# Optimization experiments

Measured on AMD Instinct MI355X. Metric: run time of the kernel, lower is better.

The kernel has to match this reference:

```python
import jax, jax.numpy as jnp
import numpy as np

NEG_SLOPE = 0.2  # LeakyReLU slope

N, E, D_IN, D_OUT, H, NBIN = 50000, 500000, 256, 256, 8, 10
DH = D_OUT // H


def setup_inputs() -> dict:
    key = jax.random.key(0)
    ks = jax.random.split(key, 9)
    emb_rel = jax.random.normal(ks[0], (N, D_IN), dtype=jnp.float32)
    head_idxs = jax.random.randint(ks[1], (E,), 0, N, dtype=jnp.int32)
    tail_idxs = jax.random.randint(ks[2], (E,), 0, N, dtype=jnp.int32)
    bins = jax.random.randint(ks[3], (E,), 0, NBIN, dtype=jnp.int32)
    # xavier-normal-ish scaled params (gain for relu)
    attn_proj_w = jax.random.normal(ks[4], (D_OUT, 2 * D_IN), dtype=jnp.float32) * (1.4142 * (2.0 / (2 * D_IN + D_OUT)) ** 0.5)
    attn_proj_b = jnp.zeros((D_OUT,), dtype=jnp.float32)
    attn_bin = jax.random.normal(ks[5], (NBIN, H, 1), dtype=jnp.float32) * 0.3
    attn_vec = jax.random.normal(ks[6], (1, H, DH), dtype=jnp.float32) * (1.4142 * (2.0 / (H + DH)) ** 0.5)
    aggr_proj_w = jax.random.normal(ks[7], (D_OUT, D_IN), dtype=jnp.float32) * (1.4142 * (2.0 / (D_IN + D_OUT)) ** 0.5)
    aggr_proj_b = jnp.zeros((D_OUT,), dtype=jnp.float32)
    return {
        "emb_rel": emb_rel,
        "head_idxs": head_idxs,
        "tail_idxs": tail_idxs,
        "bins": bins,
        "attn_proj_w": attn_proj_w,
        "attn_proj_b": attn_proj_b,
        "attn_bin": attn_bin,
        "attn_vec": attn_vec,
        "aggr_proj_w": aggr_proj_w,
        "aggr_proj_b": aggr_proj_b,
        "num_nodes": N,
    }


def reference(emb_rel, head_idxs, tail_idxs, bins, attn_proj_w, attn_proj_b,
              attn_bin, attn_vec, aggr_proj_w, aggr_proj_b, num_nodes):
    num_head, dim_hid = attn_vec.shape[1], attn_vec.shape[2]
    eh = emb_rel[head_idxs]                      # (E, D_in)
    et = emb_rel[tail_idxs]                      # (E, D_in)
    concat = jnp.concatenate([eh, et], axis=-1)  # (E, 2*D_in)
    proj = (concat @ attn_proj_w.T + attn_proj_b).reshape(-1, num_head, dim_hid)
    lrelu = jnp.where(proj >= 0, proj, NEG_SLOPE * proj)
    # raw attention logits per edge/head: (E, H, 1)
    attn_raw = jnp.sum(lrelu * attn_vec, axis=-1, keepdims=True) + attn_bin[bins]
    # segmented softmax over edges grouped by head node
    seg_max = jax.ops.segment_max(attn_raw, head_idxs, num_segments=num_nodes)
    seg_max = jnp.where(jnp.isfinite(seg_max), seg_max, 0.0)  # empty segments -> 0 (never gathered anyway)
    attn_val = jnp.exp(attn_raw - seg_max[head_idxs])
    attn_sums = jax.ops.segment_sum(attn_val, head_idxs, num_segments=num_nodes)
    beta = attn_val / (attn_sums[head_idxs] + 1e-16)            # (E, H, 1)
    aggr = (et @ aggr_proj_w.T + aggr_proj_b).reshape(-1, num_head, dim_hid)
    out = jax.ops.segment_sum(beta * aggr, head_idxs, num_segments=num_nodes)
    return out.reshape(num_nodes, num_head * dim_hid)
```

## Files before the change

### kernel.cpp

```cpp
#include <hip/hip_runtime.h>
#include <math.h>

#define D_IN 256
#define D_OUT 256
#define NH 8
#define DH 32
#define NBIN 10
#define NEG_SLOPE 0.2f
#define CAP 96
#define LOG2E 1.4426950408889634f
#define THR 8.0f

typedef short short8 __attribute__((ext_vector_type(8)));
typedef float f32x4 __attribute__((ext_vector_type(4)));

__device__ __forceinline__ unsigned short f2bf(float f) {
  unsigned u = __float_as_uint(f);
  unsigned r = u + 0x7fffu + ((u >> 16) & 1u);
  return (unsigned short)(r >> 16);
}
__device__ __forceinline__ float bf2f(unsigned short s) {
  return __uint_as_float((unsigned)s << 16);
}

__device__ __forceinline__ void gload16(const void* g, void* l) {
  __builtin_amdgcn_global_load_lds(
      (const __attribute__((address_space(1))) unsigned int*)g,
      (__attribute__((address_space(3))) unsigned int*)l, 16, 0, 0);
}

__global__ void prep_kernel(const float* __restrict__ attn_w,
                            const float* __restrict__ attn_b,
                            const float* __restrict__ aggr_w,
                            const float* __restrict__ aggr_b,
                            const float* __restrict__ emb,
                            unsigned short* __restrict__ WCbf,
                            float* __restrict__ biasC,
                            unsigned short* __restrict__ embbf,
                            int* __restrict__ cnt, int N) {
  const int b = blockIdx.x, k = threadIdx.x;
  if (b < 768) {
    const int j = b;
    int idx0 = j * 256 + k;
    if (idx0 < N) cnt[idx0] = 0;
    float v, bia = 0.f;
    if (j < 256) {
      v = attn_w[j * 512 + k];
    } else {
      int idx = j - 256, g = idx >> 3, r = idx & 7;
      if (r < 4) { int c = g * 4 + r;     v = attn_w[c * 512 + 256 + k]; bia = attn_b[c]; }
      else       { int c = g * 4 + r - 4; v = aggr_w[c * 256 + k];       bia = aggr_b[c]; }
    }
    WCbf[j * 256 + k] = f2bf(v);
    if (k == 0) biasC[j] = bia;
  } else {
    const long long total = (long long)N * 256;
    long long i = (((long long)(b - 768)) * 256 + k) * 8;
    if (i >= total) return;
    float4 a = *(const float4*)(emb + i);
    float4 c = *(const float4*)(emb + i + 4);
    short8 o;
    o[0] = (short)f2bf(a.x); o[1] = (short)f2bf(a.y);
    o[2] = (short)f2bf(a.z); o[3] = (short)f2bf(a.w);
    o[4] = (short)f2bf(c.x); o[5] = (short)f2bf(c.y);
    o[6] = (short)f2bf(c.z); o[7] = (short)f2bf(c.w);
    *(short8*)(embbf + i) = o;
  }
}

#define EPAD 36
__global__ __launch_bounds__(256) void gemm_bf16_kernel(
    const unsigned short* __restrict__ Abf,
    const unsigned short* __restrict__ Bbf,
    const float* __restrict__ biasC,
    float* __restrict__ P1, unsigned short* __restrict__ P2A, int N) {
  __shared__ char smem[32768];
  float* Ls = (float*)smem;
  const int tid = threadIdx.x;
  const int row0 = blockIdx.x * 128, col0 = blockIdx.y * 128;
  const int wave = tid >> 6, l = tid & 63;
  const int wm = wave >> 1, wn = wave & 1;
  const int lr = l & 15;
  const int lq = l >> 4;
  const int srow = tid >> 2;
  const int sk = (tid & 3) * 8;
  int ar0 = row0 + srow;      if (ar0 >= N) ar0 = N - 1;
  int ar1 = row0 + 64 + srow; if (ar1 >= N) ar1 = N - 1;
  const unsigned short* pa0 = Abf + (size_t)ar0 * 256 + sk;
  const unsigned short* pa1 = Abf + (size_t)ar1 * 256 + sk;
  const unsigned short* pb0 = Bbf + (size_t)(col0 + srow) * 256 + sk;
  const unsigned short* pb1 = Bbf + (size_t)(col0 + 64 + srow) * 256 + sk;

  auto STAGE = [&](int buf, int kk) {
    unsigned short* base = (unsigned short*)(smem + buf * 16384);
    gload16(pa0 + kk, base + wave * 512);
    gload16(pa1 + kk, base + 2048 + wave * 512);
    gload16(pb0 + kk, base + 4096 + wave * 512);
    gload16(pb1 + kk, base + 6144 + wave * 512);
  };

  f32x4 acc[4][4] = {};
  STAGE(0, 0);
  __syncthreads();
  int cur = 0;
  for (int t = 0; t < 8; ++t) {
    if (t < 7) STAGE(cur ^ 1, (t + 1) * 32);
    __builtin_amdgcn_sched_barrier(0);
    const unsigned short* As = (const unsigned short*)(smem + cur * 16384);
    const unsigned short* Bs = As + 4096;
    short8 af[4], bfr[4];
#pragma unroll
    for (int i = 0; i < 4; ++i)
      af[i] = *(const short8*)&As[(wm * 64 + i * 16 + lr) * 32 + lq * 8];
#pragma unroll
    for (int j = 0; j < 4; ++j)
      bfr[j] = *(const short8*)&Bs[(wn * 64 + j * 16 + lr) * 32 + lq * 8];
#pragma unroll
    for (int i = 0; i < 4; ++i)
#pragma unroll
      for (int j = 0; j < 4; ++j)
        acc[i][j] = __builtin_amdgcn_mfma_f32_16x16x32_bf16(af[i], bfr[j], acc[i][j], 0, 0, 0);
    __syncthreads();
    cur ^= 1;
  }
  for (int j = 0; j < 4; ++j) {
    __syncthreads();
    const float bias = biasC[col0 + wn * 64 + j * 16 + lr];
#pragma unroll
    for (int i = 0; i < 4; ++i) {
      const int lrow = wm * 64 + i * 16 + lq * 4;
#pragma unroll
      for (int r = 0; r < 4; ++r)
        Ls[(lrow + r) * EPAD + wn * 16 + lr] = acc[i][j][r] + bias;
    }
    __syncthreads();
    if (col0 < 256) {
      const int sub = tid & 7, half = sub >> 2, quad = sub & 3;
#pragma unroll
      for (int s = 0; s < 4; ++s) {
        const int row = (tid >> 3) + s * 32;
        const int grow = row0 + row;
        if (grow < N) {
          float4 v = *(const float4*)&Ls[row * EPAD + half * 16 + quad * 4];
          *(float4*)(P1 + (size_t)grow * 256 + col0 + half * 64 + j * 16 + quad * 4) = v;
        }
      }
    } else {
      const int o = tid & 3, half = o >> 1, part = o & 1;
#pragma unroll
      for (int s = 0; s < 2; ++s) {
        const int row = (tid >> 2) + s * 64;
        const int grow = row0 + row;
        if (grow < N) {
          const float* src = &Ls[row * EPAD + half * 16 + part * 8];
          short8 v;
#pragma unroll
          for (int q = 0; q < 8; ++q) v[q] = (short)f2bf(src[q]);
          *(short8*)(P2A + (size_t)grow * 512 + (col0 - 256) + half * 64 + j * 16 + part * 8) = v;
        }
      }
    }
  }
}

__global__ void bucket_scatter_kernel(const int* __restrict__ head,
                                      const int* __restrict__ tail,
                                      const int* __restrict__ bins,
                                      int* __restrict__ cnt,
                                      int* __restrict__ bucket, int E) {
  int e = blockIdx.x * blockDim.x + threadIdx.x;
  if (e >= E) return;
  int h = head[e];
  int slot = atomicAdd(&cnt[h], 1);
  if (slot < CAP) bucket[(size_t)h * CAP + slot] = (bins[e] << 16) | tail[e];
}

template <int PAT>
__device__ __forceinline__ float swz_add(float s) {
  return s + __uint_as_float(
      (unsigned)__builtin_amdgcn_ds_swizzle((int)__float_as_uint(s), PAT));
}

__device__ __forceinline__ short8 ldP2A(const unsigned short* __restrict__ P2A,
                                        int t, int l8) {
  return *(const short8*)(P2A + ((size_t)(t & 0xFFFF) << 9) + l8);
}

__device__ __forceinline__ float edge_dot(short8 c, float4 p1, float4 av) {
  float x, s;
  x = p1.x + bf2f((unsigned short)c[0]); s  = fmaxf(x, NEG_SLOPE * x) * av.x;
  x = p1.y + bf2f((unsigned short)c[1]); s += fmaxf(x, NEG_SLOPE * x) * av.y;
  x = p1.z + bf2f((unsigned short)c[2]); s += fmaxf(x, NEG_SLOPE * x) * av.z;
  x = p1.w + bf2f((unsigned short)c[3]); s += fmaxf(x, NEG_SLOPE * x) * av.w;
  s = swz_add<0x041F>(s);
  s = swz_add<0x081F>(s);
  s = swz_add<0x101F>(s);
  return s;
}

__device__ __forceinline__ float4 edge_val(short8 c) {
  float4 v;
  v.x = bf2f((unsigned short)c[4]); v.y = bf2f((unsigned short)c[5]);
  v.z = bf2f((unsigned short)c[6]); v.w = bf2f((unsigned short)c[7]);
  return v;
}

__global__ __launch_bounds__(128) void node_aggr_kernel(
    const float* __restrict__ P1, const unsigned short* __restrict__ P2A,
    const int* __restrict__ cnt, const int* __restrict__ bucket,
    const float* __restrict__ attn_vec, const float* __restrict__ attn_bin,
    float* __restrict__ out, int N) {
  __shared__ float sbin[NBIN * NH];
  const int tid = threadIdx.x;
  if (tid < NBIN * NH) sbin[tid] = attn_bin[tid] * LOG2E;
  __syncthreads();
  const int nu = __builtin_amdgcn_readfirstlane(blockIdx.x * 2 + (tid >> 6));
  if (nu >= N) return;
  const int l = tid & 63;
  const int l8 = l * 8;
  const int h = l >> 3;
  float4 av = *(const float4*)(attn_vec + l * 4);
  av.x *= LOG2E; av.y *= LOG2E; av.z *= LOG2E; av.w *= LOG2E;
  const float4 p1 = *(const float4*)(P1 + (size_t)nu * 256 + l * 4);
  const int* brow = bucket + (size_t)nu * CAP;
  int d = cnt[nu];
  if (d > CAP) d = CAP;
  float m = 0.f, m8 = 0.f, sum = 0.f;
  float4 acc = make_float4(0.f, 0.f, 0.f, 0.f);
  if (d > 0) {
    const int dm1 = d - 1;
    const int t0 = brow[0];
    short8 c0 = ldP2A(P2A, t0, l8);
    int ta[4];
    short8 ca[4];
#pragma unroll
    for (int k = 0; k < 4; ++k) {
      const int ja = (1 + k <= dm1) ? 1 + k : dm1;
      ta[k] = brow[ja];
      ca[k] = ldP2A(P2A, ta[k], l8);
    }
    __builtin_amdgcn_sched_barrier(0);
    m = edge_dot(c0, p1, av) + sbin[(t0 >> 16) * NH + h];
    m8 = m + THR;
    sum = 1.f;
    const float4 v0 = edge_val(c0);
    acc.x = v0.x; acc.y = v0.y; acc.z = v0.z; acc.w = v0.w;
    int i = 1;
#pragma unroll 2
    for (; i + 3 < d; i += 4) {
      int tn[4];
      short8 cn[4];
#pragma unroll
      for (int k = 0; k < 4; ++k) {
        const int jn = (i + 4 + k <= dm1) ? i + 4 + k : dm1;
        tn[k] = brow[jn];
        cn[k] = ldP2A(P2A, tn[k], l8);
      }
      __builtin_amdgcn_sched_barrier(0);
      float lg[4];
#pragma unroll
      for (int k = 0; k < 4; ++k)
        lg[k] = edge_dot(ca[k], p1, av) + sbin[(ta[k] >> 16) * NH + h];
      const float lmax = fmaxf(fmaxf(lg[0], lg[1]), fmaxf(lg[2], lg[3]));
      if (__any(lmax > m8)) {
        const float mn = fmaxf(m, lmax);
        const float sc = __builtin_amdgcn_exp2f(m - mn);
        sum *= sc; acc.x *= sc; acc.y *= sc; acc.z *= sc; acc.w *= sc;
        m = mn; m8 = mn + THR;
      }
#pragma unroll
      for (int k = 0; k < 4; ++k) {
        const float w = __builtin_amdgcn_exp2f(lg[k] - m);
        const float4 v = edge_val(ca[k]);
        sum += w;
        acc.x += w * v.x; acc.y += w * v.y;
        acc.z += w * v.z; acc.w += w * v.w;
      }
#pragma unroll
      for (int k = 0; k < 4; ++k) { ta[k] = tn[k]; ca[k] = cn[k]; }
    }
    const int r = d - i;
#pragma unroll
    for (int k = 0; k < 3; ++k) {
      if (k < r) {
        const float lgk = edge_dot(ca[k], p1, av) + sbin[(ta[k] >> 16) * NH + h];
        if (__any(lgk > m8)) {
          const float mn = fmaxf(m, lgk);
          const float sc = __builtin_amdgcn_exp2f(m - mn);
          sum *= sc; acc.x *= sc; acc.y *= sc; acc.z *= sc; acc.w *= sc;
          m = mn; m8 = mn + THR;
        }
        const float w = __builtin_amdgcn_exp2f(lgk - m);
        const float4 v = edge_val(ca[k]);
        sum += w;
        acc.x += w * v.x; acc.y += w * v.y;
        acc.z += w * v.z; acc.w += w * v.w;
      }
    }
  }
  const float inv = 1.f / (sum + 1e-16f);
  float4 o;
  o.x = acc.x * inv; o.y = acc.y * inv; o.z = acc.z * inv; o.w = acc.w * inv;
  *(float4*)(out + (size_t)nu * 256 + l * 4) = o;
}

extern "C" void kernel_launch(void* const* d_in, const int* in_sizes, int n_in,
                              void* d_out, int out_size, void* d_ws, size_t ws_size,
                              hipStream_t stream) {
  const float* emb      = (const float*)d_in[0];
  const int*   head     = (const int*)d_in[1];
  const int*   tail     = (const int*)d_in[2];
  const int*   bins     = (const int*)d_in[3];
  const float* attn_w   = (const float*)d_in[4];
  const float* attn_b   = (const float*)d_in[5];
  const float* attn_bin = (const float*)d_in[6];
  const float* attn_vec = (const float*)d_in[7];
  const float* aggr_w   = (const float*)d_in[8];
  const float* aggr_b   = (const float*)d_in[9];
  float* out = (float*)d_out;

  const int N = in_sizes[0] / D_IN;
  const int E = in_sizes[1];

  char* ws = (char*)d_ws;
  size_t off = 0;
  auto walloc = [&](size_t bytes) -> void* {
    void* p = ws + off;
    off += (bytes + 255) & ~(size_t)255;
    return p;
  };
  float*          P1     = (float*)walloc((size_t)N * 256 * sizeof(float));
  unsigned short* P2A    = (unsigned short*)walloc((size_t)N * 512 * sizeof(short));
  unsigned short* embbf  = (unsigned short*)walloc((size_t)N * 256 * sizeof(short));
  unsigned short* WCbf   = (unsigned short*)walloc((size_t)768 * 256 * sizeof(short));
  float*          biasC  = (float*)walloc(768 * sizeof(float));
  int*            cnt    = (int*)walloc((size_t)N * sizeof(int));
  int*            bucket = (int*)walloc((size_t)N * CAP * sizeof(int));

  const int conv_blocks = (int)(((long long)N * 256 / 8 + 255) / 256);
  prep_kernel<<<768 + conv_blocks, 256, 0, stream>>>(attn_w, attn_b, aggr_w, aggr_b,
                                                     emb, WCbf, biasC, embbf, cnt, N);

  dim3 ggrid((N + 127) / 128, 768 / 128);
  gemm_bf16_kernel<<<ggrid, 256, 0, stream>>>(embbf, WCbf, biasC, P1, P2A, N);

  bucket_scatter_kernel<<<(E + 255) / 256, 256, 0, stream>>>(head, tail, bins, cnt, bucket, E);

  node_aggr_kernel<<<(N + 1) / 2, 128, 0, stream>>>(P1, P2A, cnt, bucket,
                                                    attn_vec, attn_bin, out, N);
}
```

Before: 294.8 us.

## Stage gathered edge rows through LDS with async global-to-LDS double buffering

Replaces the register-based 4-edge prefetch in the node aggregation kernel with direct global-to-LDS loads (gload16). Edges are processed in pairs through a two-stage LDS ring per wave, with explicit vmcnt and lgkmcnt waits. It also drops the peeled first edge by starting the running max at a very negative value. The aim is to cut register pressure and keep gathers in flight, at the cost of fewer outstanding loads per wave (4 edges instead of up to 8) plus extra LDS round trips and wait instructions.

```diff
diff --git a/kernel.cpp b/kernel.cpp
--- a/kernel.cpp
+++ b/kernel.cpp
@@ -181,11 +181,6 @@
       (unsigned)__builtin_amdgcn_ds_swizzle((int)__float_as_uint(s), PAT));
 }
 
-__device__ __forceinline__ short8 ldP2A(const unsigned short* __restrict__ P2A,
-                                        int t, int l8) {
-  return *(const short8*)(P2A + ((size_t)(t & 0xFFFF) << 9) + l8);
-}
-
 __device__ __forceinline__ float edge_dot(short8 c, float4 p1, float4 av) {
   float x, s;
   x = p1.x + bf2f((unsigned short)c[0]); s  = fmaxf(x, NEG_SLOPE * x) * av.x;
@@ -211,91 +206,77 @@
     const float* __restrict__ attn_vec, const float* __restrict__ attn_bin,
     float* __restrict__ out, int N) {
   __shared__ float sbin[NBIN * NH];
+  __shared__ short stage[2][2][2][512];
   const int tid = threadIdx.x;
   if (tid < NBIN * NH) sbin[tid] = attn_bin[tid] * LOG2E;
   __syncthreads();
-  const int nu = __builtin_amdgcn_readfirstlane(blockIdx.x * 2 + (tid >> 6));
+  const int wv = tid >> 6;
+  const int nu = __builtin_amdgcn_readfirstlane(blockIdx.x * 2 + wv);
   if (nu >= N) return;
   const int l = tid & 63;
-  const int l8 = l * 8;
+  const int l16 = l * 16;
   const int h = l >> 3;
   float4 av = *(const float4*)(attn_vec + l * 4);
   av.x *= LOG2E; av.y *= LOG2E; av.z *= LOG2E; av.w *= LOG2E;
   const float4 p1 = *(const float4*)(P1 + (size_t)nu * 256 + l * 4);
+  asm volatile("s_waitcnt vmcnt(0)" ::: "memory");
+  __builtin_amdgcn_sched_barrier(0);
   const int* brow = bucket + (size_t)nu * CAP;
   int d = cnt[nu];
   if (d > CAP) d = CAP;
-  float m = 0.f, m8 = 0.f, sum = 0.f;
+  float m = -3.0e38f, m8 = -3.0e38f, sum = 0.f;
   float4 acc = make_float4(0.f, 0.f, 0.f, 0.f);
   if (d > 0) {
     const int dm1 = d - 1;
-    const int t0 = brow[0];
-    short8 c0 = ldP2A(P2A, t0, l8);
-    int ta[4];
-    short8 ca[4];
-#pragma unroll
-    for (int k = 0; k < 4; ++k) {
-      const int ja = (1 + k <= dm1) ? 1 + k : dm1;
-      ta[k] = brow[ja];
-      ca[k] = ldP2A(P2A, ta[k], l8);
-    }
-    __builtin_amdgcn_sched_barrier(0);
-    m = edge_dot(c0, p1, av) + sbin[(t0 >> 16) * NH + h];
-    m8 = m + THR;
-    sum = 1.f;
-    const float4 v0 = edge_val(c0);
-    acc.x = v0.x; acc.y = v0.y; acc.z = v0.z; acc.w = v0.w;
-    int i = 1;
-#pragma unroll 2
-    for (; i + 3 < d; i += 4) {
-      int tn[4];
-      short8 cn[4];
-#pragma unroll
-      for (int k = 0; k < 4; ++k) {
-        const int jn = (i + 4 + k <= dm1) ? i + 4 + k : dm1;
-        tn[k] = brow[jn];
-        cn[k] = ldP2A(P2A, tn[k], l8);
+    const int P = (d + 1) >> 1;
+    char* lb0 = (char*)&stage[wv][0][0][0];
+    char* lb1 = (char*)&stage[wv][1][0][0];
+    int tc0 = brow[0];
+    int tc1 = brow[1 <= dm1 ? 1 : dm1];
+    int tn0 = brow[2 <= dm1 ? 2 : dm1];
+    int tn1 = brow[3 <= dm1 ? 3 : dm1];
+    gload16(P2A + ((size_t)(tc0 & 0xFFFF) << 9) + l * 8, lb0);
+    gload16(P2A + ((size_t)(tc1 & 0xFFFF) << 9) + l * 8, lb0 + 1024);
+    if (P > 1) {
+      gload16(P2A + ((size_t)(tn0 & 0xFFFF) << 9) + l * 8, lb1);
+      gload16(P2A + ((size_t)(tn1 & 0xFFFF) << 9) + l * 8, lb1 + 1024);
+    }
+    for (int p = 0; p < P; ++p) {
+      const int j2 = 2 * (p + 2);
+      const int tf0 = brow[j2 <= dm1 ? j2 : dm1];
+      const int tf1 = brow[j2 + 1 <= dm1 ? j2 + 1 : dm1];
+      if (p + 1 < P) { asm volatile("s_waitcnt vmcnt(2)" ::: "memory"); }
+      else           { asm volatile("s_waitcnt vmcnt(0)" ::: "memory"); }
+      __builtin_amdgcn_sched_barrier(0);
+      char* lb = (p & 1) ? lb1 : lb0;
+      const short8 c0 = *(const short8*)(lb + l16);
+      const short8 c1 = *(const short8*)(lb + 1024 + l16);
+      asm volatile("s_waitcnt lgkmcnt(0)" ::: "memory");
+      __builtin_amdgcn_sched_barrier(0);
+      if (p + 2 < P) {
+        gload16(P2A + ((size_t)(tf0 & 0xFFFF) << 9) + l * 8, lb);
+        gload16(P2A + ((size_t)(tf1 & 0xFFFF) << 9) + l * 8, lb + 1024);
       }
       __builtin_amdgcn_sched_barrier(0);
-      float lg[4];
-#pragma unroll
-      for (int k = 0; k < 4; ++k)
-        lg[k] = edge_dot(ca[k], p1, av) + sbin[(ta[k] >> 16) * NH + h];
-      const float lmax = fmaxf(fmaxf(lg[0], lg[1]), fmaxf(lg[2], lg[3]));
+      const float l0 = edge_dot(c0, p1, av) + sbin[(tc0 >> 16) * NH + h];
+      float l1 = edge_dot(c1, p1, av) + sbin[(tc1 >> 16) * NH + h];
+      if (2 * p + 1 > dm1) l1 = -3.0e38f;
+      const float lmax = fmaxf(l0, l1);
       if (__any(lmax > m8)) {
         const float mn = fmaxf(m, lmax);
         const float sc = __builtin_amdgcn_exp2f(m - mn);
         sum *= sc; acc.x *= sc; acc.y *= sc; acc.z *= sc; acc.w *= sc;
         m = mn; m8 = mn + THR;
       }
-#pragma unroll
-      for (int k = 0; k < 4; ++k) {
-        const float w = __builtin_amdgcn_exp2f(lg[k] - m);
-        const float4 v = edge_val(ca[k]);
-        sum += w;
-        acc.x += w * v.x; acc.y += w * v.y;
-        acc.z += w * v.z; acc.w += w * v.w;
-      }
-#pragma unroll
-      for (int k = 0; k < 4; ++k) { ta[k] = tn[k]; ca[k] = cn[k]; }
-    }
-    const int r = d - i;
-#pragma unroll
-    for (int k = 0; k < 3; ++k) {
-      if (k < r) {
-        const float lgk = edge_dot(ca[k], p1, av) + sbin[(ta[k] >> 16) * NH + h];
-        if (__any(lgk > m8)) {
-          const float mn = fmaxf(m, lgk);
-          const float sc = __builtin_amdgcn_exp2f(m - mn);
-          sum *= sc; acc.x *= sc; acc.y *= sc; acc.z *= sc; acc.w *= sc;
-          m = mn; m8 = mn + THR;
-        }
-        const float w = __builtin_amdgcn_exp2f(lgk - m);
-        const float4 v = edge_val(ca[k]);
-        sum += w;
-        acc.x += w * v.x; acc.y += w * v.y;
-        acc.z += w * v.z; acc.w += w * v.w;
-      }
+      const float w0 = __builtin_amdgcn_exp2f(l0 - m);
+      const float w1 = __builtin_amdgcn_exp2f(l1 - m);
+      sum += w0 + w1;
+      const float4 v0 = edge_val(c0), v1 = edge_val(c1);
+      acc.x += w0 * v0.x + w1 * v1.x;
+      acc.y += w0 * v0.y + w1 * v1.y;
+      acc.z += w0 * v0.z + w1 * v1.z;
+      acc.w += w0 * v0.w + w1 * v1.w;
+      tc0 = tn0; tc1 = tn1; tn0 = tf0; tn1 = tf1;
     }
   }
   const float inv = 1.f / (sum + 1e-16f);
```

Result: no change. 293.9 us (-0.3%).
